# Performance work log

Measured on AMD Instinct MI355X. Metric: run time of the kernel, lower is better.

## Reference

```python
import jax, jax.numpy as jnp
import numpy as np

N_NODES = 100000


def _mean_agg(feat, src, dst, n):
    # segment mean of neighbor messages: h_N[v] = mean_{(u->v) in E} feat[u]
    s = jax.ops.segment_sum(feat[src], dst, num_segments=n)  # [n, d]
    cnt = jax.ops.segment_sum(jnp.ones_like(src, dtype=feat.dtype), dst, num_segments=n)
    return s / jnp.maximum(cnt, 1.0)[:, None]  # isolated nodes -> 0 (DGL mean gives 0)


def setup_inputs() -> dict:
    key = jax.random.key(0)
    k1, k2, k3, k4, k5 = jax.random.split(key, 5)
    n, d_in, d_hid, d_out, n_edges = N_NODES, 128, 128, 64, 1600000
    feat = jax.random.normal(k1, (n, d_in), dtype=jnp.float32)
    edge_src = jax.random.randint(k2, (n_edges,), 0, n, dtype=jnp.int32)
    edge_dst = jax.random.randint(k3, (n_edges,), 0, n, dtype=jnp.int32)
    # xavier_uniform with relu gain, torch Linear weight layout [out, in]
    gain = float(np.sqrt(2.0))
    def xavier(k, out_f, in_f):
        bound = gain * np.sqrt(6.0 / (in_f + out_f))
        return jax.random.uniform(k, (out_f, in_f), minval=-bound, maxval=bound, dtype=jnp.float32)
    W0 = xavier(k4, d_hid, 2 * d_in)
    W1 = xavier(k5, d_out, 2 * d_hid)
    return {"feat": feat, "edge_src": edge_src, "edge_dst": edge_dst, "W0": W0, "W1": W1}


def reference(feat, edge_src, edge_dst, W0, W1):
    n = feat.shape[0]
    # layer 0: mean-aggregate, concat, linear, relu (dropout p=0 -> identity)
    h_N = _mean_agg(feat, edge_src, edge_dst, n)
    h = jax.nn.relu(jnp.concatenate([feat, h_N], axis=1) @ W0.T)
    # final layer: mean-aggregate, concat, linear (no relu)
    h_N2 = _mean_agg(h, edge_src, edge_dst, n)
    out = jnp.concatenate([h, h_N2], axis=1) @ W1.T
    return out
```

## Files before the change

kernel.cpp:

```cpp
#include <hip/hip_runtime.h>
#include <hip/hip_bf16.h>

typedef __attribute__((ext_vector_type(8))) short bf16x8;
typedef __attribute__((ext_vector_type(4))) float f32x4;
typedef __attribute__((ext_vector_type(2))) float f32x2;

#define BSH 9
#define BCAP 12288

#if __has_builtin(__builtin_amdgcn_cvt_pk_f32_fp8) && __has_builtin(__builtin_amdgcn_cvt_pk_fp8_f32)
#define FP8_HW 1
#else
#define FP8_HW 0
#endif

__device__ __forceinline__ float bf2f(unsigned short u) {
    return __uint_as_float(((unsigned int)u) << 16);
}
__device__ __forceinline__ unsigned short f2bf(float f) {
    unsigned int u = __float_as_uint(f);
    unsigned int r = u + 0x7FFFu + ((u >> 16) & 1u);
    return (unsigned short)(r >> 16);
}
__device__ __forceinline__ unsigned int pack2bf(float a, float b) {
    return (unsigned int)f2bf(a) | ((unsigned int)f2bf(b) << 16);
}

#if !FP8_HW
__device__ __forceinline__ unsigned int f2fp8_sw(float v) {
    unsigned int u = __float_as_uint(v);
    unsigned int s = (u >> 24) & 0x80u;
    unsigned int a = u & 0x7FFFFFFFu;
    float av = __uint_as_float(a);
    unsigned int q;
    if (av >= 0.015625f) {
        unsigned int r = a + 0x7FFFFu + ((a >> 20) & 1u);
        q = (r - (120u << 23)) >> 20;
        if (q > 0x7Eu) q = 0x7Eu;
    } else {
        q = (unsigned int)(av * 512.0f + 0.5f);
    }
    return s | q;
}
__device__ __forceinline__ float fp8_dec_sw(unsigned int u8) {
    unsigned int s = (u8 & 0x80u) << 24;
    unsigned int em = u8 & 0x7Fu;
    float vn = __uint_as_float(s | ((em << 20) + (120u << 23)));
    float vs = __uint_as_float(s | 0x3B000000u) * (float)(int)em;
    return em >= 8 ? vn : vs;
}
#endif

__device__ __forceinline__ void fp8x4_dec(unsigned int d, float& x, float& y, float& z, float& w) {
#if FP8_HW
    f32x2 lo = __builtin_amdgcn_cvt_pk_f32_fp8((int)d, false);
    f32x2 hi = __builtin_amdgcn_cvt_pk_f32_fp8((int)d, true);
    x = lo.x; y = lo.y; z = hi.x; w = hi.y;
#else
    x = fp8_dec_sw(d & 0xFFu);
    y = fp8_dec_sw((d >> 8) & 0xFFu);
    z = fp8_dec_sw((d >> 16) & 0xFFu);
    w = fp8_dec_sw((d >> 24) & 0xFFu);
#endif
}
__device__ __forceinline__ unsigned int fp8x4_enc(float a, float b, float c, float d) {
#if FP8_HW
    int u = __builtin_amdgcn_cvt_pk_fp8_f32(a, b, 0, false);
    u = __builtin_amdgcn_cvt_pk_fp8_f32(c, d, u, true);
    return (unsigned int)u;
#else
    return f2fp8_sw(a) | (f2fp8_sw(b) << 8) | (f2fp8_sw(c) << 16) | (f2fp8_sw(d) << 24);
#endif
}

__global__ __launch_bounds__(256) void megaA(const int* __restrict__ esrc, const int* __restrict__ edst,
                                             int* __restrict__ gcur, unsigned int* __restrict__ pairs,
                                             int E, int NB,
                                             const float* __restrict__ feat, unsigned short* __restrict__ Fb,
                                             unsigned char* __restrict__ Ff8, int nquad,
                                             const float* __restrict__ W0, unsigned short* __restrict__ Wb1,
                                             const float* __restrict__ W1, unsigned short* __restrict__ Wb2,
                                             int pblocks, int cblocks) {
    __shared__ int bcnt[256];
    __shared__ int bbas[256];
    int b = blockIdx.x, t = threadIdx.x;
    if (b < pblocks) {
        int e0 = b * 4096;
        int eend = min(e0 + 4096, E);
        if (t < NB) bcnt[t] = 0;
        __syncthreads();
        for (int e = e0 + t; e < eend; e += 256) atomicAdd(&bcnt[edst[e] >> BSH], 1);
        __syncthreads();
        if (t < NB) {
            bbas[t] = t * BCAP + atomicAdd(&gcur[t], bcnt[t]);
            bcnt[t] = 0;
        }
        __syncthreads();
        for (int e = e0 + t; e < eend; e += 256) {
            int d = edst[e];
            int s = esrc[e];
            int bk = d >> BSH;
            int off = atomicAdd(&bcnt[bk], 1);
            pairs[bbas[bk] + off] = (unsigned int)s | ((unsigned int)(d & ((1 << BSH) - 1)) << 17);
        }
    } else if (b < pblocks + cblocks) {
        int cb = b - pblocks;
        for (int q = cb * 256 + t; q < nquad; q += cblocks * 256) {
            float4 f = *(const float4*)(feat + (size_t)q * 4);
            ushort4 ub;
            ub.x = f2bf(f.x); ub.y = f2bf(f.y); ub.z = f2bf(f.z); ub.w = f2bf(f.w);
            *(ushort4*)(Fb + (size_t)q * 4) = ub;
            *(unsigned int*)(Ff8 + (size_t)q * 4) = fp8x4_enc(f.x, f.y, f.z, f.w);
        }
    } else {
        int wb = b - pblocks - cblocks;
        for (int i = wb * 256 + t; i < 49152; i += 24 * 256) {
            if (i < 32768) {
                Wb1[i] = f2bf(W0[i]);
            } else {
                int i2 = i - 32768;
                int j = i2 >> 7, k = i2 & 127;
                float vv = (j < 64) ? W1[j * 256 + k] : W1[(j - 64) * 256 + 128 + k];
                Wb2[i2] = f2bf(vv);
            }
        }
    }
}

__global__ __launch_bounds__(256) void build(const unsigned int* __restrict__ pairs,
                                             const int* __restrict__ gcur,
                                             int* __restrict__ offs, int* __restrict__ csr,
                                             int n, int NB, int E) {
    __shared__ int cnt[512];
    __shared__ int excl[512];
    __shared__ int wsum[4];
    __shared__ int woff[4];
    __shared__ int sbase;
    int b = blockIdx.x, t = threadIdx.x, lane = t & 63, wv = t >> 6;

    {
        int vv = (t < NB) ? gcur[t] : 0;
        int x = vv;
#pragma unroll
        for (int o = 1; o < 64; o <<= 1) {
            int y = __shfl_up(x, o, 64);
            if (lane >= o) x += y;
        }
        if (lane == 63) wsum[wv] = x;
        __syncthreads();
        if (t == 0) {
            int r = 0;
            for (int w = 0; w < 4; ++w) { woff[w] = r; r += wsum[w]; }
        }
        __syncthreads();
        if (t == b) sbase = woff[wv] + x - vv;
        if (b == 0 && t == 0) offs[n] = E;
    }
    __syncthreads();
    int base = sbase;
    int p0 = b * BCAP;
    int m = gcur[b];
    int v0 = b << BSH;

    cnt[t] = 0;
    cnt[t + 256] = 0;
    __syncthreads();
    for (int i = t; i < m; i += 256) atomicAdd(&cnt[pairs[p0 + i] >> 17], 1);
    __syncthreads();
    int c0 = cnt[2 * t], c1 = cnt[2 * t + 1];
    int s = c0 + c1;
    int x = s;
#pragma unroll
    for (int o = 1; o < 64; o <<= 1) {
        int y = __shfl_up(x, o, 64);
        if (lane >= o) x += y;
    }
    if (lane == 63) wsum[wv] = x;
    __syncthreads();
    if (t == 0) {
        int r = 0;
        for (int w = 0; w < 4; ++w) { woff[w] = r; r += wsum[w]; }
    }
    __syncthreads();
    int ex = woff[wv] + x - s;
    excl[2 * t] = ex;
    excl[2 * t + 1] = ex + c0;
    int v = v0 + 2 * t;
    if (v + 1 < n) {
        int2 o2;
        o2.x = base + ex;
        o2.y = base + ex + c0;
        *(int2*)(offs + v) = o2;
    } else if (v < n) {
        offs[v] = base + ex;
    }
    cnt[t] = 0;
    cnt[t + 256] = 0;
    __syncthreads();
    for (int i = t; i < m; i += 256) {
        unsigned int u = pairs[p0 + i];
        int dl = u >> 17;
        int off = atomicAdd(&cnt[dl], 1);
        csr[base + excl[dl] + off] = (int)(u & 0x1FFFFu);
    }
}

__global__ __launch_bounds__(256) void agg1(const unsigned char* __restrict__ Ff8,
                                            const int* __restrict__ offs,
                                            const int* __restrict__ csr,
                                            unsigned short* __restrict__ Mb, int n) {
    int t = threadIdx.x;
    int q = t >> 4, cl = t & 15;
    int v = blockIdx.x * 16 + q;
    if (v >= n) return;
    int beg = offs[v], end = offs[v + 1];
    float a0 = 0.f, a1 = 0.f, a2 = 0.f, a3 = 0.f;
    float a4 = 0.f, a5 = 0.f, a6 = 0.f, a7 = 0.f;
    int e = beg;
    for (; e + 7 < end; e += 8) {
        int s[8];
#pragma unroll
        for (int k = 0; k < 8; ++k) s[k] = csr[e + k];
        uint2 d[8];
#pragma unroll
        for (int k = 0; k < 8; ++k)
            d[k] = *(const uint2*)(Ff8 + (size_t)s[k] * 128 + cl * 8);
#pragma unroll
        for (int k = 0; k < 8; ++k) {
            float x0, y0, z0, w0, x1, y1, z1, w1;
            fp8x4_dec(d[k].x, x0, y0, z0, w0);
            fp8x4_dec(d[k].y, x1, y1, z1, w1);
            a0 += x0; a1 += y0; a2 += z0; a3 += w0;
            a4 += x1; a5 += y1; a6 += z1; a7 += w1;
        }
    }
    for (; e < end; ++e) {
        uint2 d0 = *(const uint2*)(Ff8 + (size_t)csr[e] * 128 + cl * 8);
        float x0, y0, z0, w0, x1, y1, z1, w1;
        fp8x4_dec(d0.x, x0, y0, z0, w0);
        fp8x4_dec(d0.y, x1, y1, z1, w1);
        a0 += x0; a1 += y0; a2 += z0; a3 += w0;
        a4 += x1; a5 += y1; a6 += z1; a7 += w1;
    }
    int deg = end - beg;
    float inv = 1.0f / (float)(deg > 0 ? deg : 1);
    uint4 pk;
    pk.x = pack2bf(a0 * inv, a1 * inv);
    pk.y = pack2bf(a2 * inv, a3 * inv);
    pk.z = pack2bf(a4 * inv, a5 * inv);
    pk.w = pack2bf(a6 * inv, a7 * inv);
    *(uint4*)(Mb + (size_t)v * 128 + cl * 8) = pk;
}

__global__ __launch_bounds__(256) void fused_gemm(const unsigned short* __restrict__ Fb,
                                                  const unsigned short* __restrict__ Mb,
                                                  const unsigned short* __restrict__ Wb1,
                                                  const unsigned short* __restrict__ Wc,
                                                  unsigned short* __restrict__ Za,
                                                  unsigned char* __restrict__ Zb8,
                                                  int n) {
    __shared__ __align__(16) unsigned char smem[16384];
    int t = threadIdx.x, l = t & 63, w = t >> 6;
    int lr = l & 15;
    int lk8 = (l >> 4) * 8;
    int rbase = (l >> 4) * 4;
    int m0 = blockIdx.x * 64;

    bf16x8 w1f[2][8];
#pragma unroll
    for (int of = 0; of < 2; ++of)
#pragma unroll
        for (int kc = 0; kc < 8; ++kc)
            w1f[of][kc] = *(const bf16x8*)(Wb1 + (size_t)(w * 32 + of * 16 + lr) * 256 + kc * 32 + lk8);
    bf16x8 w2f[2][4];
#pragma unroll
    for (int of = 0; of < 2; ++of)
#pragma unroll
        for (int kc = 0; kc < 4; ++kc)
            w2f[of][kc] = *(const bf16x8*)(Wc + (size_t)(w * 32 + of * 16 + lr) * 128 + kc * 32 + lk8);

    f32x4 acc[2][4];
#pragma unroll
    for (int of = 0; of < 2; ++of)
#pragma unroll
        for (int nf = 0; nf < 4; ++nf) acc[of][nf] = (f32x4){0.f, 0.f, 0.f, 0.f};
#pragma unroll
    for (int nf = 0; nf < 4; ++nf) {
        int node = m0 + nf * 16 + lr;
        node = (node < n) ? node : (n - 1);
#pragma unroll
        for (int kc = 0; kc < 8; ++kc) {
            int kb = kc * 32 + lk8;
            bf16x8 x;
            if (kb < 128)
                x = *(const bf16x8*)(Fb + (size_t)node * 128 + kb);
            else
                x = *(const bf16x8*)(Mb + (size_t)node * 128 + (kb - 128));
            acc[0][nf] = __builtin_amdgcn_mfma_f32_16x16x32_bf16(w1f[0][kc], x, acc[0][nf], 0, 0, 0);
            acc[1][nf] = __builtin_amdgcn_mfma_f32_16x16x32_bf16(w1f[1][kc], x, acc[1][nf], 0, 0, 0);
        }
    }
#pragma unroll
    for (int of = 0; of < 2; ++of)
#pragma unroll
        for (int nf = 0; nf < 4; ++nf) {
            int node = nf * 16 + lr;
            unsigned int ob = (unsigned int)((w * 32 + of * 16 + rbase) * 2);
            uint2 pk;
            pk.x = pack2bf(fmaxf(acc[of][nf][0], 0.f), fmaxf(acc[of][nf][1], 0.f));
            pk.y = pack2bf(fmaxf(acc[of][nf][2], 0.f), fmaxf(acc[of][nf][3], 0.f));
            *(uint2*)(smem + node * 256 + (ob ^ ((unsigned int)(node & 15) << 4))) = pk;
        }
    __syncthreads();

    f32x4 acc2[2][4];
#pragma unroll
    for (int of = 0; of < 2; ++of)
#pragma unroll
        for (int nf = 0; nf < 4; ++nf) acc2[of][nf] = (f32x4){0.f, 0.f, 0.f, 0.f};
#pragma unroll
    for (int nf = 0; nf < 4; ++nf) {
        int node = nf * 16 + lr;
        unsigned int sw2 = (unsigned int)(node & 15) << 4;
#pragma unroll
        for (int kc = 0; kc < 4; ++kc) {
            unsigned int kbyte = (unsigned int)((kc * 32 + lk8) * 2);
            bf16x8 x = *(const bf16x8*)(smem + node * 256 + (kbyte ^ sw2));
            acc2[0][nf] = __builtin_amdgcn_mfma_f32_16x16x32_bf16(w2f[0][kc], x, acc2[0][nf], 0, 0, 0);
            acc2[1][nf] = __builtin_amdgcn_mfma_f32_16x16x32_bf16(w2f[1][kc], x, acc2[1][nf], 0, 0, 0);
        }
    }
    __syncthreads();

    {
        unsigned char* zaT = smem;
        unsigned char* zbT = smem + 8192;
#pragma unroll
        for (int of = 0; of < 2; ++of)
#pragma unroll
            for (int nf = 0; nf < 4; ++nf) {
                int node = nf * 16 + lr;
                int out = w * 32 + of * 16 + rbase;
                if (w < 2) {
                    uint2 pk;
                    pk.x = pack2bf(acc2[of][nf][0], acc2[of][nf][1]);
                    pk.y = pack2bf(acc2[of][nf][2], acc2[of][nf][3]);
                    unsigned int ob = (unsigned int)(out * 2);
                    *(uint2*)(zaT + node * 128 + (ob ^ ((unsigned int)(node & 7) << 4))) = pk;
                } else {
                    unsigned int pk = fp8x4_enc(acc2[of][nf][0], acc2[of][nf][1],
                                                acc2[of][nf][2], acc2[of][nf][3]);
                    unsigned int ob = (unsigned int)(out - 64);
                    *(unsigned int*)(zbT + node * 64 + (ob ^ ((unsigned int)(node & 3) << 4))) = pk;
                }
            }
    }
    __syncthreads();

#pragma unroll
    for (int c = 0; c < 2; ++c) {
        int chunk = c * 256 + t;
        int row = chunk >> 3, cb = (chunk & 7) * 16;
        int grow = m0 + row;
        if (grow < n)
            *(uint4*)((unsigned char*)Za + (size_t)grow * 128 + cb) =
                *(const uint4*)(smem + row * 128 + (cb ^ ((row & 7) << 4)));
    }
    {
        int row = t >> 2, cb = (t & 3) * 16;
        int grow = m0 + row;
        if (grow < n)
            *(uint4*)(Zb8 + (size_t)grow * 64 + cb) =
                *(const uint4*)(smem + 8192 + row * 64 + (cb ^ ((row & 3) << 4)));
    }
}

__global__ __launch_bounds__(256) void agg2(const unsigned short* __restrict__ Za,
                                            const unsigned char* __restrict__ Zb8,
                                            const int* __restrict__ offs,
                                            const int* __restrict__ csr,
                                            float* __restrict__ out, int n) {
    int t = threadIdx.x;
    int q = t >> 4, cl = t & 15;
    int v = blockIdx.x * 16 + q;
    if (v >= n) return;
    int beg = offs[v], end = offs[v + 1];
    float a0 = 0.f, a1 = 0.f, a2 = 0.f, a3 = 0.f;
    int e = beg;
    for (; e + 7 < end; e += 8) {
        int s[8];
#pragma unroll
        for (int k = 0; k < 8; ++k) s[k] = csr[e + k];
        unsigned int d[8];
#pragma unroll
        for (int k = 0; k < 8; ++k)
            d[k] = *(const unsigned int*)(Zb8 + (size_t)s[k] * 64 + cl * 4);
#pragma unroll
        for (int k = 0; k < 8; ++k) {
            float x, y, z, u2;
            fp8x4_dec(d[k], x, y, z, u2);
            a0 += x; a1 += y; a2 += z; a3 += u2;
        }
    }
    for (; e < end; ++e) {
        unsigned int d0 = *(const unsigned int*)(Zb8 + (size_t)csr[e] * 64 + cl * 4);
        float x, y, z, u2;
        fp8x4_dec(d0, x, y, z, u2);
        a0 += x; a1 += y; a2 += z; a3 += u2;
    }
    int deg = end - beg;
    float inv = 1.0f / (float)(deg > 0 ? deg : 1);
    uint2 uz = *(const uint2*)((const unsigned char*)Za + (size_t)v * 128 + cl * 8);
    float4 o;
    o.x = bf2f((unsigned short)uz.x) + a0 * inv;
    o.y = bf2f((unsigned short)(uz.x >> 16)) + a1 * inv;
    o.z = bf2f((unsigned short)uz.y) + a2 * inv;
    o.w = bf2f((unsigned short)(uz.y >> 16)) + a3 * inv;
    *(float4*)(out + (size_t)v * 64 + cl * 4) = o;
}

extern "C" void kernel_launch(void* const* d_in, const int* in_sizes, int n_in,
                              void* d_out, int out_size, void* d_ws, size_t ws_size,
                              hipStream_t stream) {
    const float* feat = (const float*)d_in[0];
    const int* esrc = (const int*)d_in[1];
    const int* edst = (const int*)d_in[2];
    const float* W0 = (const float*)d_in[3];
    const float* W1 = (const float*)d_in[4];
    float* out = (float*)d_out;

    int n = in_sizes[0] / 128;
    int E = in_sizes[1];
    int NB = (n + 511) >> 9;

    char* ws = (char*)d_ws;
    size_t off = 0;
    auto alloc = [&](size_t bytes) -> void* {
        void* p = ws + off;
        off += (bytes + 255) & ~(size_t)255;
        return p;
    };
    int* offs = (int*)alloc((size_t)(n + 1) * 4);
    int* csr = (int*)alloc((size_t)E * 4);
    int* gcur = (int*)alloc((size_t)NB * 4);
    unsigned int* pairs = (unsigned int*)alloc((size_t)NB * BCAP * 4);
    unsigned short* Wb1 = (unsigned short*)alloc((size_t)128 * 256 * 2);
    unsigned short* Wb2 = (unsigned short*)alloc((size_t)128 * 128 * 2);
    unsigned short* Fb = (unsigned short*)alloc((size_t)n * 128 * 2);
    unsigned char* Ff8 = (unsigned char*)alloc((size_t)n * 128);
    unsigned short* Mb = (unsigned short*)alloc((size_t)n * 128 * 2);
    unsigned short* Za = (unsigned short*)alloc((size_t)n * 64 * 2);
    unsigned char* Zb8 = (unsigned char*)alloc((size_t)n * 64);

    int pblocks = (E + 4095) / 4096;
    int cblocks = 640;
    int nquad = n * 32;

    hipMemsetAsync(gcur, 0, (size_t)NB * 4, stream);
    megaA<<<pblocks + cblocks + 24, 256, 0, stream>>>(esrc, edst, gcur, pairs, E, NB,
                                                      feat, Fb, Ff8, nquad,
                                                      W0, Wb1, W1, Wb2, pblocks, cblocks);
    build<<<NB, 256, 0, stream>>>(pairs, gcur, offs, csr, n, NB, E);

    agg1<<<(n + 15) / 16, 256, 0, stream>>>(Ff8, offs, csr, Mb, n);
    int ntiles = (n + 63) / 64;
    fused_gemm<<<ntiles, 256, 0, stream>>>(Fb, Mb, Wb1, Wb2, Za, Zb8, n);
    agg2<<<(n + 15) / 16, 256, 0, stream>>>(Za, Zb8, offs, csr, out, n);
}
```

Baseline: 184.8 us.

## Unroll gathers by 16 with split accumulators; process two tiles per GEMM block

Result: slower. 190.9 us (+3.3%).

```diff
diff --git a/kernel.cpp b/kernel.cpp
--- a/kernel.cpp
+++ b/kernel.cpp
@@ -216,7 +216,30 @@
     int beg = offs[v], end = offs[v + 1];
     float a0 = 0.f, a1 = 0.f, a2 = 0.f, a3 = 0.f;
     float a4 = 0.f, a5 = 0.f, a6 = 0.f, a7 = 0.f;
+    float b0 = 0.f, b1 = 0.f, b2 = 0.f, b3 = 0.f;
+    float b4 = 0.f, b5 = 0.f, b6 = 0.f, b7 = 0.f;
     int e = beg;
+    for (; e + 15 < end; e += 16) {
+        int s[16];
+#pragma unroll
+        for (int k = 0; k < 16; ++k) s[k] = csr[e + k];
+        uint2 d[16];
+#pragma unroll
+        for (int k = 0; k < 16; ++k)
+            d[k] = *(const uint2*)(Ff8 + (size_t)s[k] * 128 + cl * 8);
+#pragma unroll
+        for (int k = 0; k < 16; k += 2) {
+            float x0, y0, z0, w0, x1, y1, z1, w1;
+            fp8x4_dec(d[k].x, x0, y0, z0, w0);
+            fp8x4_dec(d[k].y, x1, y1, z1, w1);
+            a0 += x0; a1 += y0; a2 += z0; a3 += w0;
+            a4 += x1; a5 += y1; a6 += z1; a7 += w1;
+            fp8x4_dec(d[k + 1].x, x0, y0, z0, w0);
+            fp8x4_dec(d[k + 1].y, x1, y1, z1, w1);
+            b0 += x0; b1 += y0; b2 += z0; b3 += w0;
+            b4 += x1; b5 += y1; b6 += z1; b7 += w1;
+        }
+    }
     for (; e + 7 < end; e += 8) {
         int s[8];
 #pragma unroll
@@ -242,6 +265,8 @@
         a0 += x0; a1 += y0; a2 += z0; a3 += w0;
         a4 += x1; a5 += y1; a6 += z1; a7 += w1;
     }
+    a0 += b0; a1 += b1; a2 += b2; a3 += b3;
+    a4 += b4; a5 += b5; a6 += b6; a7 += b7;
     int deg = end - beg;
     float inv = 1.0f / (float)(deg > 0 ? deg : 1);
     uint4 pk;
@@ -258,13 +283,12 @@
                                                   const unsigned short* __restrict__ Wc,
                                                   unsigned short* __restrict__ Za,
                                                   unsigned char* __restrict__ Zb8,
-                                                  int n) {
+                                                  int n, int ntiles) {
     __shared__ __align__(16) unsigned char smem[16384];
     int t = threadIdx.x, l = t & 63, w = t >> 6;
     int lr = l & 15;
     int lk8 = (l >> 4) * 8;
     int rbase = (l >> 4) * 4;
-    int m0 = blockIdx.x * 64;
 
     bf16x8 w1f[2][8];
 #pragma unroll
@@ -279,99 +303,107 @@
         for (int kc = 0; kc < 4; ++kc)
             w2f[of][kc] = *(const bf16x8*)(Wc + (size_t)(w * 32 + of * 16 + lr) * 128 + kc * 32 + lk8);
 
-    f32x4 acc[2][4];
-#pragma unroll
-    for (int of = 0; of < 2; ++of)
-#pragma unroll
-        for (int nf = 0; nf < 4; ++nf) acc[of][nf] = (f32x4){0.f, 0.f, 0.f, 0.f};
-#pragma unroll
-    for (int nf = 0; nf < 4; ++nf) {
-        int node = m0 + nf * 16 + lr;
-        node = (node < n) ? node : (n - 1);
-#pragma unroll
-        for (int kc = 0; kc < 8; ++kc) {
-            int kb = kc * 32 + lk8;
-            bf16x8 x;
-            if (kb < 128)
-                x = *(const bf16x8*)(Fb + (size_t)node * 128 + kb);
-            else
-                x = *(const bf16x8*)(Mb + (size_t)node * 128 + (kb - 128));
-            acc[0][nf] = __builtin_amdgcn_mfma_f32_16x16x32_bf16(w1f[0][kc], x, acc[0][nf], 0, 0, 0);
-            acc[1][nf] = __builtin_amdgcn_mfma_f32_16x16x32_bf16(w1f[1][kc], x, acc[1][nf], 0, 0, 0);
-        }
-    }
-#pragma unroll
-    for (int of = 0; of < 2; ++of)
+#pragma unroll 1
+    for (int it = 0; it < 2; ++it) {
+        int tile = blockIdx.x * 2 + it;
+        if (tile >= ntiles) break;
+        int m0 = tile * 64;
+
+        f32x4 acc[2][4];
+#pragma unroll
+        for (int of = 0; of < 2; ++of)
+#pragma unroll
+            for (int nf = 0; nf < 4; ++nf) acc[of][nf] = (f32x4){0.f, 0.f, 0.f, 0.f};
+#pragma unroll
+        for (int nf = 0; nf < 4; ++nf) {
+            int node = m0 + nf * 16 + lr;
+            node = (node < n) ? node : (n - 1);
+#pragma unroll
+            for (int kc = 0; kc < 8; ++kc) {
+                int kb = kc * 32 + lk8;
+                bf16x8 x;
+                if (kb < 128)
+                    x = *(const bf16x8*)(Fb + (size_t)node * 128 + kb);
+                else
+                    x = *(const bf16x8*)(Mb + (size_t)node * 128 + (kb - 128));
+                acc[0][nf] = __builtin_amdgcn_mfma_f32_16x16x32_bf16(w1f[0][kc], x, acc[0][nf], 0, 0, 0);
+                acc[1][nf] = __builtin_amdgcn_mfma_f32_16x16x32_bf16(w1f[1][kc], x, acc[1][nf], 0, 0, 0);
+            }
+        }
+#pragma unroll
+        for (int of = 0; of < 2; ++of)
+#pragma unroll
+            for (int nf = 0; nf < 4; ++nf) {
+                int node = nf * 16 + lr;
+                unsigned int ob = (unsigned int)((w * 32 + of * 16 + rbase) * 2);
+                uint2 pk;
+                pk.x = pack2bf(fmaxf(acc[of][nf][0], 0.f), fmaxf(acc[of][nf][1], 0.f));
+                pk.y = pack2bf(fmaxf(acc[of][nf][2], 0.f), fmaxf(acc[of][nf][3], 0.f));
+                *(uint2*)(smem + node * 256 + (ob ^ ((unsigned int)(node & 15) << 4))) = pk;
+            }
+        __syncthreads();
+
+        f32x4 acc2[2][4];
+#pragma unroll
+        for (int of = 0; of < 2; ++of)
+#pragma unroll
+            for (int nf = 0; nf < 4; ++nf) acc2[of][nf] = (f32x4){0.f, 0.f, 0.f, 0.f};
 #pragma unroll
         for (int nf = 0; nf < 4; ++nf) {
             int node = nf * 16 + lr;
-            unsigned int ob = (unsigned int)((w * 32 + of * 16 + rbase) * 2);
-            uint2 pk;
-            pk.x = pack2bf(fmaxf(acc[of][nf][0], 0.f), fmaxf(acc[of][nf][1], 0.f));
-            pk.y = pack2bf(fmaxf(acc[of][nf][2], 0.f), fmaxf(acc[of][nf][3], 0.f));
-            *(uint2*)(smem + node * 256 + (ob ^ ((unsigned int)(node & 15) << 4))) = pk;
-        }
-    __syncthreads();
-
-    f32x4 acc2[2][4];
-#pragma unroll
-    for (int of = 0; of < 2; ++of)
-#pragma unroll
-        for (int nf = 0; nf < 4; ++nf) acc2[of][nf] = (f32x4){0.f, 0.f, 0.f, 0.f};
-#pragma unroll
-    for (int nf = 0; nf < 4; ++nf) {
-        int node = nf * 16 + lr;
-        unsigned int sw2 = (unsigned int)(node & 15) << 4;
-#pragma unroll
-        for (int kc = 0; kc < 4; ++kc) {
-            unsigned int kbyte = (unsigned int)((kc * 32 + lk8) * 2);
-            bf16x8 x = *(const bf16x8*)(smem + node * 256 + (kbyte ^ sw2));
-            acc2[0][nf] = __builtin_amdgcn_mfma_f32_16x16x32_bf16(w2f[0][kc], x, acc2[0][nf], 0, 0, 0);
-            acc2[1][nf] = __builtin_amdgcn_mfma_f32_16x16x32_bf16(w2f[1][kc], x, acc2[1][nf], 0, 0, 0);
-        }
-    }
-    __syncthreads();
-
-    {
-        unsigned char* zaT = smem;
-        unsigned char* zbT = smem + 8192;
-#pragma unroll
-        for (int of = 0; of < 2; ++of)
-#pragma unroll
-            for (int nf = 0; nf < 4; ++nf) {
-                int node = nf * 16 + lr;
-                int out = w * 32 + of * 16 + rbase;
-                if (w < 2) {
-                    uint2 pk;
-                    pk.x = pack2bf(acc2[of][nf][0], acc2[of][nf][1]);
-                    pk.y = pack2bf(acc2[of][nf][2], acc2[of][nf][3]);
-                    unsigned int ob = (unsigned int)(out * 2);
-                    *(uint2*)(zaT + node * 128 + (ob ^ ((unsigned int)(node & 7) << 4))) = pk;
-                } else {
-                    unsigned int pk = fp8x4_enc(acc2[of][nf][0], acc2[of][nf][1],
-                                                acc2[of][nf][2], acc2[of][nf][3]);
-                    unsigned int ob = (unsigned int)(out - 64);
-                    *(unsigned int*)(zbT + node * 64 + (ob ^ ((unsigned int)(node & 3) << 4))) = pk;
+            unsigned int sw2 = (unsigned int)(node & 15) << 4;
+#pragma unroll
+            for (int kc = 0; kc < 4; ++kc) {
+                unsigned int kbyte = (unsigned int)((kc * 32 + lk8) * 2);
+                bf16x8 x = *(const bf16x8*)(smem + node * 256 + (kbyte ^ sw2));
+                acc2[0][nf] = __builtin_amdgcn_mfma_f32_16x16x32_bf16(w2f[0][kc], x, acc2[0][nf], 0, 0, 0);
+                acc2[1][nf] = __builtin_amdgcn_mfma_f32_16x16x32_bf16(w2f[1][kc], x, acc2[1][nf], 0, 0, 0);
+            }
+        }
+        __syncthreads();
+
+        {
+            unsigned char* zaT = smem;
+            unsigned char* zbT = smem + 8192;
+#pragma unroll
+            for (int of = 0; of < 2; ++of)
+#pragma unroll
+                for (int nf = 0; nf < 4; ++nf) {
+                    int node = nf * 16 + lr;
+                    int out = w * 32 + of * 16 + rbase;
+                    if (w < 2) {
+                        uint2 pk;
+                        pk.x = pack2bf(acc2[of][nf][0], acc2[of][nf][1]);
+                        pk.y = pack2bf(acc2[of][nf][2], acc2[of][nf][3]);
+                        unsigned int ob = (unsigned int)(out * 2);
+                        *(uint2*)(zaT + node * 128 + (ob ^ ((unsigned int)(node & 7) << 4))) = pk;
+                    } else {
+                        unsigned int pk = fp8x4_enc(acc2[of][nf][0], acc2[of][nf][1],
+                                                    acc2[of][nf][2], acc2[of][nf][3]);
+                        unsigned int ob = (unsigned int)(out - 64);
+                        *(unsigned int*)(zbT + node * 64 + (ob ^ ((unsigned int)(node & 3) << 4))) = pk;
+                    }
                 }
-            }
-    }
-    __syncthreads();
-
-#pragma unroll
-    for (int c = 0; c < 2; ++c) {
-        int chunk = c * 256 + t;
-        int row = chunk >> 3, cb = (chunk & 7) * 16;
-        int grow = m0 + row;
-        if (grow < n)
-            *(uint4*)((unsigned char*)Za + (size_t)grow * 128 + cb) =
-                *(const uint4*)(smem + row * 128 + (cb ^ ((row & 7) << 4)));
-    }
-    {
-        int row = t >> 2, cb = (t & 3) * 16;
-        int grow = m0 + row;
-        if (grow < n)
-            *(uint4*)(Zb8 + (size_t)grow * 64 + cb) =
-                *(const uint4*)(smem + 8192 + row * 64 + (cb ^ ((row & 3) << 4)));
+        }
+        __syncthreads();
+
+#pragma unroll
+        for (int c = 0; c < 2; ++c) {
+            int chunk = c * 256 + t;
+            int row = chunk >> 3, cb = (chunk & 7) * 16;
+            int grow = m0 + row;
+            if (grow < n)
+                *(uint4*)((unsigned char*)Za + (size_t)grow * 128 + cb) =
+                    *(const uint4*)(smem + row * 128 + (cb ^ ((row & 7) << 4)));
+        }
+        {
+            int row = t >> 2, cb = (t & 3) * 16;
+            int grow = m0 + row;
+            if (grow < n)
+                *(uint4*)(Zb8 + (size_t)grow * 64 + cb) =
+                    *(const uint4*)(smem + 8192 + row * 64 + (cb ^ ((row & 3) << 4)));
+        }
+        __syncthreads();
     }
 }
 
@@ -386,7 +418,25 @@
     if (v >= n) return;
     int beg = offs[v], end = offs[v + 1];
     float a0 = 0.f, a1 = 0.f, a2 = 0.f, a3 = 0.f;
+    float b0 = 0.f, b1 = 0.f, b2 = 0.f, b3 = 0.f;
     int e = beg;
+    for (; e + 15 < end; e += 16) {
+        int s[16];
+#pragma unroll
+        for (int k = 0; k < 16; ++k) s[k] = csr[e + k];
+        unsigned int d[16];
+#pragma unroll
+        for (int k = 0; k < 16; ++k)
+            d[k] = *(const unsigned int*)(Zb8 + (size_t)s[k] * 64 + cl * 4);
+#pragma unroll
+        for (int k = 0; k < 16; k += 2) {
+            float x, y, z, u2;
+            fp8x4_dec(d[k], x, y, z, u2);
+            a0 += x; a1 += y; a2 += z; a3 += u2;
+            fp8x4_dec(d[k + 1], x, y, z, u2);
+            b0 += x; b1 += y; b2 += z; b3 += u2;
+        }
+    }
     for (; e + 7 < end; e += 8) {
         int s[8];
 #pragma unroll
@@ -408,6 +458,7 @@
         fp8x4_dec(d0, x, y, z, u2);
         a0 += x; a1 += y; a2 += z; a3 += u2;
     }
+    a0 += b0; a1 += b1; a2 += b2; a3 += b3;
     int deg = end - beg;
     float inv = 1.0f / (float)(deg > 0 ? deg : 1);
     uint2 uz = *(const uint2*)((const unsigned char*)Za + (size_t)v * 128 + cl * 8);
@@ -464,6 +515,6 @@
 
     agg1<<<(n + 15) / 16, 256, 0, stream>>>(Ff8, offs, csr, Mb, n);
     int ntiles = (n + 63) / 64;
-    fused_gemm<<<ntiles, 256, 0, stream>>>(Fb, Mb, Wb1, Wb2, Za, Zb8, n);
+    fused_gemm<<<(ntiles + 1) / 2, 256, 0, stream>>>(Fb, Mb, Wb1, Wb2, Za, Zb8, n, ntiles);
     agg2<<<(n + 15) / 16, 256, 0, stream>>>(Za, Zb8, offs, csr, out, n);
 }
```
